# Performance work log

Hardware: AMD Instinct MI355X
Metric: run time of the kernel (lower is better)

The kernel has to match this reference:

```python
import jax, jax.numpy as jnp
import numpy as np

B, L, P, K, D, H = 8192, 224, 6, 5, 128, 4
S = K * K                 # 25 spatial positions in the patch
CENTER = S // 2           # central target pixel index
SCALE_RANGE = 0.2
BN_EPS = 1e-5


def _uniform(k, shape, fan_in):
    s = 1.0 / np.sqrt(fan_in)
    return jax.random.uniform(k, shape, jnp.float32, -s, s)


def setup_inputs() -> dict:
    key = jax.random.key(0)
    ks = jax.random.split(key, 32)
    inp = {}
    inp["x"] = jax.random.normal(ks[0], (B, L, K, K), jnp.float32)
    # attention projections (stored as (in, out), applied as x @ W + b)
    inp["wk_w"] = _uniform(ks[1], (L, D), L); inp["wk_b"] = _uniform(ks[2], (D,), L)
    inp["wv_w"] = _uniform(ks[3], (L, D), L); inp["wv_b"] = _uniform(ks[4], (D,), L)
    inp["wq_w"] = _uniform(ks[5], (L, D), L); inp["wq_b"] = _uniform(ks[6], (D,), L)
    inp["ng_w"] = _uniform(ks[7], (D, 1), D); inp["ng_b"] = _uniform(ks[8], (1,), D)
    # ffn branch: GLU(128->64) -> BN -> GLU(64->P)
    inp["f1_fw"] = _uniform(ks[9], (D, 64), D);  inp["f1_fb"] = _uniform(ks[10], (64,), D)
    inp["f1_gw"] = _uniform(ks[11], (D, 64), D); inp["f1_gb"] = _uniform(ks[12], (64,), D)
    inp["f_bn_g"] = jnp.ones((64,), jnp.float32); inp["f_bn_b"] = jnp.zeros((64,), jnp.float32)
    inp["f2_fw"] = _uniform(ks[13], (64, P), 64); inp["f2_fb"] = _uniform(ks[14], (P,), 64)
    inp["f2_gw"] = _uniform(ks[15], (64, P), 64); inp["f2_gb"] = _uniform(ks[16], (P,), 64)
    # scalar branch: same shapes
    inp["s1_fw"] = _uniform(ks[17], (D, 64), D);  inp["s1_fb"] = _uniform(ks[18], (64,), D)
    inp["s1_gw"] = _uniform(ks[19], (D, 64), D);  inp["s1_gb"] = _uniform(ks[20], (64,), D)
    inp["s_bn_g"] = jnp.ones((64,), jnp.float32); inp["s_bn_b"] = jnp.zeros((64,), jnp.float32)
    inp["s2_fw"] = _uniform(ks[21], (64, P), 64); inp["s2_fb"] = _uniform(ks[22], (P,), 64)
    inp["s2_gw"] = _uniform(ks[23], (64, P), 64); inp["s2_gb"] = _uniform(ks[24], (P,), 64)
    # endmember spectra (P, L), nonnegative as typical for HSI
    inp["endmember"] = jax.random.uniform(ks[25], (P, L), jnp.float32)
    return inp


def _swish(x):
    return x * jax.nn.sigmoid(x)


def _glu(x, fw, fb, gw, gb):
    return (x @ fw + fb) * jax.nn.sigmoid(x @ gw + gb)


def _bn_train(x, g, b):
    # BatchNorm1d training-mode forward: biased batch stats over batch dim
    m = jnp.mean(x, axis=0)
    v = jnp.var(x, axis=0)
    return (x - m) * jax.lax.rsqrt(v + BN_EPS) * g + b


def _forward(x, wk_w, wk_b, wv_w, wv_b, wq_w, wq_b, ng_w, ng_b,
             f1_fw, f1_fb, f1_gw, f1_gb, f_bn_g, f_bn_b, f2_fw, f2_fb, f2_gw, f2_gb,
             s1_fw, s1_fb, s1_gw, s1_gb, s_bn_g, s_bn_b, s2_fw, s2_fb, s2_gw, s2_gb,
             endmember):
    b = x.shape[0]
    xt = x.reshape(b, L, S).transpose(0, 2, 1)        # (B, S, L)
    keys = xt @ wk_w + wk_b                            # (B, S, D)
    vals = xt @ wv_w + wv_b                            # (B, S, D)
    q = xt[:, CENTER] @ wq_w + wq_b                    # (B, D)
    dk, dv = D // H, D // H
    kh = keys.reshape(b, S, H, dk)
    qh = q.reshape(b, H, dk)
    # note: scaling uses full key_dim (np.sqrt(self.key_dim)), not per-head dim
    scores = jnp.einsum('bhd,bshd->bhs', qh, kh) / np.sqrt(D).astype(np.float32)
    mask = jnp.zeros((S,), jnp.float32).at[CENTER].set(-1e6)
    att = jax.nn.softmax(scores + mask, axis=-1)       # (B, H, S)
    vh = vals.reshape(b, S, H, dv)
    surround = jnp.einsum('bhs,bshd->bhd', att, vh).reshape(b, D)
    central = vals[:, CENTER]                          # (B, D)
    nearby = jax.nn.sigmoid((central - surround) @ ng_w + ng_b)  # (B, 1)
    ss = central + nearby * surround                   # (B, D) spatial-spectral feature

    h = _glu(_swish(ss), f1_fw, f1_fb, f1_gw, f1_gb)
    h = _swish(_bn_train(h, f_bn_g, f_bn_b))
    abd = jax.nn.softmax(_glu(h, f2_fw, f2_fb, f2_gw, f2_gb), axis=1)  # (B, P)

    g = _glu(_swish(ss), s1_fw, s1_fb, s1_gw, s1_gb)
    g = _swish(_bn_train(g, s_bn_g, s_bn_b))
    edm_scale = jnp.tanh(_glu(g, s2_fw, s2_fb, s2_gw, s2_gb))          # (B, P)

    scale = 1.0 + SCALE_RANGE * edm_scale[:, :, None]  # (B, P, 1)
    edm = scale * endmember[None]                      # (B, P, L)
    recon = jnp.einsum('bp,bpl->bl', abd, edm)         # (B, L)
    return recon, abd, edm_scale


def reference(x, wk_w, wk_b, wv_w, wv_b, wq_w, wq_b, ng_w, ng_b,
              f1_fw, f1_fb, f1_gw, f1_gb, f_bn_g, f_bn_b, f2_fw, f2_fb, f2_gw, f2_gb,
              s1_fw, s1_fb, s1_gw, s1_gb, s_bn_g, s_bn_b, s2_fw, s2_fb, s2_gw, s2_gb,
              endmember):
    return _forward(x, wk_w, wk_b, wv_w, wv_b, wq_w, wq_b, ng_w, ng_b,
                    f1_fw, f1_fb, f1_gw, f1_gb, f_bn_g, f_bn_b, f2_fw, f2_fb, f2_gw, f2_gb,
                    s1_fw, s1_fb, s1_gw, s1_gb, s_bn_g, s_bn_b, s2_fw, s2_fb, s2_gw, s2_gb,
                    endmember)
```

## Files before the change

kernel.cpp:

```cpp
#include <hip/hip_runtime.h>
#include <hip/hip_bf16.h>

typedef unsigned short ushort;
typedef unsigned int   uint;
typedef __bf16 bfrag_t __attribute__((ext_vector_type(8)));
typedef float  ffrag_t __attribute__((ext_vector_type(4)));

#define NB   8192
#define LL   224
#define SS   25
#define CTR  12
#define DD   128
#define PP   6
#define HID  64
#define GPB  2
#define NGRP 4
#define NKC  7
#define NMT  4
#define NNT  24
#define VST  132
#define VBASE (GPB * SS * VST)
#define WPK_ELEMS (NKC * NNT * 64 * 8)
#define FC1_ELEMS (4 * 16 * 64 * 8)

__device__ __forceinline__ float f_sigmoid(float x) { return 1.0f / (1.0f + __expf(-x)); }
__device__ __forceinline__ ushort f2bf(float f) {
    __hip_bfloat16 h = __float2bfloat16(f);
    ushort u; __builtin_memcpy(&u, &h, 2); return u;
}
__device__ __forceinline__ float bfu2f(ushort u) {
    uint v = ((uint)u) << 16; float f; __builtin_memcpy(&f, &v, 4); return f;
}

__global__ __launch_bounds__(256) void k0_pack(
    const float* __restrict__ wk_w, const float* __restrict__ wv_w,
    const float* __restrict__ wq_w,
    const float* __restrict__ f1_fw, const float* __restrict__ f1_gw,
    const float* __restrict__ s1_fw, const float* __restrict__ s1_gw,
    ushort* __restrict__ wpack, ushort* __restrict__ fc1pack,
    float* __restrict__ stats)
{
    const int blk = blockIdx.x;
    if (blk == 0) stats[threadIdx.x] = 0.f;
    if (blk < NNT) {
        const int nt  = blk;
        const int mat = nt >> 3;
        const float* w = mat == 0 ? wk_w : (mat == 1 ? wv_w : wq_w);
        const int cb = (nt & 7) * 16;
        for (int e = threadIdx.x; e < NKC * 64 * 8; e += 256) {
            int j    = e & 7;
            int lane = (e >> 3) & 63;
            int kc   = e >> 9;
            int k = kc * 32 + ((lane >> 4) << 3) + j;
            int c = cb + (lane & 15);
            wpack[((kc * NNT + nt) * 64 + lane) * 8 + j] = f2bf(w[k * DD + c]);
        }
    } else {
        const int nt = blk - NNT;
        const int m2 = nt >> 2;
        const float* w = m2 == 0 ? f1_fw : (m2 == 1 ? f1_gw : (m2 == 2 ? s1_fw : s1_gw));
        const int cb = (nt & 3) * 16;
        for (int e = threadIdx.x; e < 4 * 64 * 8; e += 256) {
            int j    = e & 7;
            int lane = (e >> 3) & 63;
            int kc   = e >> 9;
            int k = kc * 32 + ((lane >> 4) << 3) + j;
            int c = cb + (lane & 15);
            fc1pack[((kc * 16 + nt) * 64 + lane) * 8 + j] = f2bf(w[k * HID + c]);
        }
    }
}

__global__ __launch_bounds__(512, 2) void kA_front(
    const float* __restrict__ x,
    const ushort* __restrict__ wpack,
    const float* __restrict__ wk_b, const float* __restrict__ wv_b,
    const float* __restrict__ wq_b,
    const float* __restrict__ ng_w, const float* __restrict__ ng_b,
    ushort* __restrict__ swv_ws)
{
    __shared__ ushort alds[NMT * NKC * 64 * 8];
    __shared__ float  qv[GPB * DD];
    __shared__ float  att[8 * 26];
    __shared__ float  red[4];

    const int t    = threadIdx.x;
    const int wave = t >> 6;
    const int lane = t & 63;

    const int cC = wave * 16 + (lane & 15);
    const float biask = wk_b[cC];
    const float biasv = wv_b[cC];
    const float biasq = wq_b[cC];
    const float ngw   = ng_w[t & 127];

    float4 xf[6];
    {
        const float4* xb4 = (const float4*)(x + (size_t)(blockIdx.x * NGRP) * GPB * (LL * SS));
#pragma unroll
        for (int k = 0; k < 6; ++k) {
            int q = t + k * 512;
            if (q < 2800) xf[k] = xb4[q];
        }
    }

    for (int j = 0; j < NGRP; ++j) {
        const int b0 = (blockIdx.x * NGRP + j) * GPB;

#pragma unroll
        for (int k = 0; k < 6; ++k) {
            int q = t + k * 512;
            if (q < 2800) {
                int e0 = q * 4;
                int g  = e0 >= 5600;
                int eb0 = e0 - g * 5600;
                int l0 = eb0 / 25;
                int s0 = eb0 - l0 * 25;
#pragma unroll
                for (int c = 0; c < 4; ++c) {
                    int s = s0 + c;
                    int l = l0;
                    if (s >= 25) { s -= 25; ++l; }
                    int r = g * 32 + s;
                    int idx = (((r >> 4) * NKC + (l >> 5)) * 64 +
                               ((r & 15) | (((l >> 3) & 3) << 4))) * 8 + (l & 7);
                    float fv = c == 0 ? xf[k].x : c == 1 ? xf[k].y : c == 2 ? xf[k].z : xf[k].w;
                    alds[idx] = f2bf(fv);
                }
            }
        }
        __syncthreads();

        ffrag_t acck[NMT], accv[NMT], accq[2];
#pragma unroll
        for (int mt = 0; mt < NMT; ++mt) {
            acck[mt] = ffrag_t{0.f, 0.f, 0.f, 0.f};
            accv[mt] = ffrag_t{0.f, 0.f, 0.f, 0.f};
        }
        accq[0] = ffrag_t{0.f, 0.f, 0.f, 0.f};
        accq[1] = ffrag_t{0.f, 0.f, 0.f, 0.f};

        bfrag_t bk = *(const bfrag_t*)(wpack + ((0 * NNT + wave) * 64 + lane) * 8);
        bfrag_t bv = *(const bfrag_t*)(wpack + ((0 * NNT + wave + 8) * 64 + lane) * 8);
        bfrag_t bq = *(const bfrag_t*)(wpack + ((0 * NNT + wave + 16) * 64 + lane) * 8);
#pragma unroll
        for (int kc = 0; kc < NKC; ++kc) {
            bfrag_t nbk, nbv, nbq;
            if (kc + 1 < NKC) {
                nbk = *(const bfrag_t*)(wpack + (((kc + 1) * NNT + wave) * 64 + lane) * 8);
                nbv = *(const bfrag_t*)(wpack + (((kc + 1) * NNT + wave + 8) * 64 + lane) * 8);
                nbq = *(const bfrag_t*)(wpack + (((kc + 1) * NNT + wave + 16) * 64 + lane) * 8);
            }
#pragma unroll
            for (int mt = 0; mt < NMT; ++mt) {
                bfrag_t af = *(const bfrag_t*)(alds + ((mt * NKC + kc) * 64 + lane) * 8);
                acck[mt] = __builtin_amdgcn_mfma_f32_16x16x32_bf16(af, bk, acck[mt], 0, 0, 0);
                accv[mt] = __builtin_amdgcn_mfma_f32_16x16x32_bf16(af, bv, accv[mt], 0, 0, 0);
                if ((mt & 1) == 0)
                    accq[mt >> 1] = __builtin_amdgcn_mfma_f32_16x16x32_bf16(af, bq, accq[mt >> 1], 0, 0, 0);
            }
            if (kc + 1 < NKC) { bk = nbk; bv = nbv; bq = nbq; }
        }
        __syncthreads();

        {
#pragma unroll
            for (int mt = 0; mt < NMT; ++mt) {
#pragma unroll
                for (int reg = 0; reg < 4; ++reg) {
                    int r = mt * 16 + ((lane >> 4) << 2) + reg;
                    int g = r >> 5;
                    int s = r & 31;
                    if (s < SS) {
                        alds[(g * SS + s) * VST + cC]         = f2bf(acck[mt][reg] + biask);
                        alds[VBASE + (g * SS + s) * VST + cC] = f2bf(accv[mt][reg] + biasv);
                    }
                }
            }
            if ((lane >> 4) == 3) {
                qv[cC]      = accq[0][0] + biasq;
                qv[DD + cC] = accq[1][0] + biasq;
            }
        }
        __syncthreads();

        if (j + 1 < NGRP) {
            const float4* xb4 = (const float4*)(x + (size_t)(b0 + GPB) * (LL * SS));
#pragma unroll
            for (int k = 0; k < 6; ++k) {
                int q = t + k * 512;
                if (q < 2800) xf[k] = xb4[q];
            }
        }

        {
            const int r    = t >> 6;
            const int g    = r >> 2;
            const int h    = r & 3;
            const int l32  = lane & 31;
            const int half = lane >> 5;
            float part = 0.f;
            if (l32 < SS) {
                const ushort* kr = alds + (g * SS + l32) * VST + h * 32 + half * 16;
                const float*  qr = qv + g * DD + h * 32 + half * 16;
                float a0 = 0.f, a1 = 0.f, a2 = 0.f, a3 = 0.f;
#pragma unroll
                for (int i = 0; i < 16; i += 4) {
                    a0 = fmaf(qr[i + 0], bfu2f(kr[i + 0]), a0);
                    a1 = fmaf(qr[i + 1], bfu2f(kr[i + 1]), a1);
                    a2 = fmaf(qr[i + 2], bfu2f(kr[i + 2]), a2);
                    a3 = fmaf(qr[i + 3], bfu2f(kr[i + 3]), a3);
                }
                part = (a0 + a1) + (a2 + a3);
            }
            part += __shfl_xor(part, 32);
            float sc = -1e30f;
            if (l32 < SS) {
                sc = part * 0.088388347648318447f;
                if (l32 == CTR) sc -= 1e6f;
            }
            float mx = sc;
#pragma unroll
            for (int m = 16; m > 0; m >>= 1) mx = fmaxf(mx, __shfl_xor(mx, m, 32));
            float e = __expf(sc - mx);
            float sum = e;
#pragma unroll
            for (int m = 16; m > 0; m >>= 1) sum += __shfl_xor(sum, m, 32);
            if (half == 0 && l32 < SS) att[r * 26 + l32] = e / sum;
        }
        __syncthreads();

        if (t < 256) {
            const int g = t >> 7;
            const int d = t & 127;
            const int h = d >> 5;
            const ushort* vrow = alds + VBASE + g * SS * VST + d;
            const float* arow = att + (g * 4 + h) * 26;
            float s0 = 0.f, s1 = 0.f;
#pragma unroll
            for (int s = 0; s < 24; s += 2) {
                s0 = fmaf(arow[s],     bfu2f(vrow[s * VST]),       s0);
                s1 = fmaf(arow[s + 1], bfu2f(vrow[(s + 1) * VST]), s1);
            }
            float sur = fmaf(arow[24], bfu2f(vrow[24 * VST]), s0 + s1);
            float cen = bfu2f(vrow[CTR * VST]);
            float term = (cen - sur) * ngw;
#pragma unroll
            for (int off = 32; off > 0; off >>= 1) term += __shfl_down(term, off);
            if (lane == 0) red[wave] = term;
            __syncthreads();
            float tot = red[g * 2] + red[g * 2 + 1] + ng_b[0];
            float nearby = f_sigmoid(tot);
            float ssv = cen + nearby * sur;
            float sw  = ssv * f_sigmoid(ssv);
            swv_ws[(size_t)(b0 + g) * DD + d] = f2bf(sw);
        } else {
            __syncthreads();
        }
    }
}

__global__ __launch_bounds__(256) void kC_fc1(
    const ushort* __restrict__ swv_ws,
    const ushort* __restrict__ fc1pack,
    const float* __restrict__ f1_fb, const float* __restrict__ f1_gb,
    const float* __restrict__ s1_fb, const float* __restrict__ s1_gb,
    float* __restrict__ h1_ws, float* __restrict__ g1_ws,
    float* __restrict__ stats)
{
    const int t    = threadIdx.x;
    const int wave = t >> 6;
    const int lane = t & 63;
    const int m0   = blockIdx.x * 32;
    const int c16  = wave * 16 + (lane & 15);

    const float fb1 = f1_fb[c16], gb1 = f1_gb[c16];
    const float fb2 = s1_fb[c16], gb2 = s1_gb[c16];

    ffrag_t acc[4][2];
#pragma unroll
    for (int ni = 0; ni < 4; ++ni)
#pragma unroll
        for (int mt = 0; mt < 2; ++mt) acc[ni][mt] = ffrag_t{0.f, 0.f, 0.f, 0.f};

#pragma unroll
    for (int kc = 0; kc < 4; ++kc) {
        bfrag_t bf[4];
#pragma unroll
        for (int ni = 0; ni < 4; ++ni) {
            int nt = wave + 4 * ni;
            bf[ni] = *(const bfrag_t*)(fc1pack + ((kc * 16 + nt) * 64 + lane) * 8);
        }
#pragma unroll
        for (int mt = 0; mt < 2; ++mt) {
            bfrag_t af = *(const bfrag_t*)(swv_ws +
                (size_t)(m0 + mt * 16 + (lane & 15)) * DD + kc * 32 + ((lane >> 4) << 3));
#pragma unroll
            for (int ni = 0; ni < 4; ++ni)
                acc[ni][mt] = __builtin_amdgcn_mfma_f32_16x16x32_bf16(af, bf[ni], acc[ni][mt], 0, 0, 0);
        }
    }

    float hs = 0.f, hq = 0.f, gs = 0.f, gq = 0.f;
#pragma unroll
    for (int mt = 0; mt < 2; ++mt) {
#pragma unroll
        for (int reg = 0; reg < 4; ++reg) {
            int m = m0 + mt * 16 + ((lane >> 4) << 2) + reg;
            float hv = (acc[0][mt][reg] + fb1) * f_sigmoid(acc[1][mt][reg] + gb1);
            float gv = (acc[2][mt][reg] + fb2) * f_sigmoid(acc[3][mt][reg] + gb2);
            h1_ws[(size_t)m * HID + c16] = hv;
            g1_ws[(size_t)m * HID + c16] = gv;
            hs += hv; hq = fmaf(hv, hv, hq);
            gs += gv; gq = fmaf(gv, gv, gq);
        }
    }
    hs += __shfl_xor(hs, 16); hs += __shfl_xor(hs, 32);
    hq += __shfl_xor(hq, 16); hq += __shfl_xor(hq, 32);
    gs += __shfl_xor(gs, 16); gs += __shfl_xor(gs, 32);
    gq += __shfl_xor(gq, 16); gq += __shfl_xor(gq, 32);
    const int cg = lane >> 4;
    float val = cg == 0 ? hs : cg == 1 ? hq : cg == 2 ? gs : gq;
    atomicAdd(&stats[cg * 64 + c16], val);
}

#define K3G 16
__global__ __launch_bounds__(256) void k3_back(
    const float* __restrict__ h1, const float* __restrict__ g1,
    const float* __restrict__ stats,
    const float* __restrict__ f_bng, const float* __restrict__ f_bnb,
    const float* __restrict__ s_bng, const float* __restrict__ s_bnb,
    const float* __restrict__ f2_fw, const float* __restrict__ f2_fb,
    const float* __restrict__ f2_gw, const float* __restrict__ f2_gb,
    const float* __restrict__ s2_fw, const float* __restrict__ s2_fb,
    const float* __restrict__ s2_gw, const float* __restrict__ s2_gb,
    const float* __restrict__ endm,
    float* __restrict__ out_recon, float* __restrict__ out_abd,
    float* __restrict__ out_es)
{
    const int B0 = blockIdx.x * K3G;
    const int t = threadIdx.x;
    __shared__ float bnl[256];
    __shared__ float w2[4][HID * PP];
    __shared__ float b2[4][8];
    __shared__ float endl[PP * LL];
    __shared__ float hh[K3G * 65], gg[K3G * 65];
    __shared__ float logit[K3G * 8], esv[K3G * 8], coef[K3G * 8];

    if (t < 128) {
        int br = t >> 6, j = t & 63;
        float S1 = stats[br * 128 + j];
        float S2 = stats[br * 128 + 64 + j];
        float m   = S1 * (1.0f / NB);
        float var = S2 * (1.0f / NB) - m * m;
        float gam = br ? s_bng[j] : f_bng[j];
        float be  = br ? s_bnb[j] : f_bnb[j];
        float a   = gam * rsqrtf(var + 1e-5f);
        bnl[br * 128 + j]      = a;
        bnl[br * 128 + 64 + j] = be - m * a;
    }
    for (int i = t; i < HID * PP; i += 256) {
        w2[0][i] = f2_fw[i];
        w2[1][i] = f2_gw[i];
        w2[2][i] = s2_fw[i];
        w2[3][i] = s2_gw[i];
    }
    if (t < PP) {
        b2[0][t] = f2_fb[t];
        b2[1][t] = f2_gb[t];
        b2[2][t] = s2_fb[t];
        b2[3][t] = s2_gb[t];
    }
    for (int i = t; i < PP * LL; i += 256) endl[i] = endm[i];
    __syncthreads();

    for (int i = t; i < K3G * HID; i += 256) {
        int ba = i >> 6, j = i & 63;
        float v1 = h1[(size_t)(B0 + ba) * HID + j] * bnl[j] + bnl[64 + j];
        hh[ba * 65 + j] = v1 * f_sigmoid(v1);
        float v2 = g1[(size_t)(B0 + ba) * HID + j] * bnl[128 + j] + bnl[192 + j];
        gg[ba * 65 + j] = v2 * f_sigmoid(v2);
    }
    __syncthreads();

    for (int i = t; i < K3G * 2 * PP; i += 256) {
        int ba = i / (2 * PP);
        int rr = i - ba * (2 * PP);
        int br = rr / PP;
        int p  = rr - br * PP;
        const float* src = (br ? gg : hh) + ba * 65;
        const float* fw  = w2[br * 2];
        const float* gw  = w2[br * 2 + 1];
        float df = b2[br * 2][p], dg = b2[br * 2 + 1][p];
#pragma unroll 8
        for (int j = 0; j < HID; ++j) {
            float v = src[j];
            df = fmaf(v, fw[j * PP + p], df);
            dg = fmaf(v, gw[j * PP + p], dg);
        }
        float glu = df * f_sigmoid(dg);
        if (br == 0) {
            logit[ba * 8 + p] = glu;
        } else {
            float e = tanhf(glu);
            esv[ba * 8 + p] = e;
            out_es[(size_t)(B0 + ba) * PP + p] = e;
        }
    }
    __syncthreads();

    if (t < K3G) {
        float mx = -1e30f;
#pragma unroll
        for (int p = 0; p < PP; ++p) mx = fmaxf(mx, logit[t * 8 + p]);
        float e[PP]; float sum = 0.f;
#pragma unroll
        for (int p = 0; p < PP; ++p) { e[p] = __expf(logit[t * 8 + p] - mx); sum += e[p]; }
        float inv = 1.0f / sum;
#pragma unroll
        for (int p = 0; p < PP; ++p) {
            float a = e[p] * inv;
            out_abd[(size_t)(B0 + t) * PP + p] = a;
            coef[t * 8 + p] = a * (1.0f + 0.2f * esv[t * 8 + p]);
        }
    }
    __syncthreads();

    for (int i = t; i < K3G * LL; i += 256) {
        int ba = i / LL;
        int l  = i - ba * LL;
        float r = 0.f;
#pragma unroll
        for (int p = 0; p < PP; ++p)
            r = fmaf(coef[ba * 8 + p], endl[p * LL + l], r);
        out_recon[(size_t)(B0 + ba) * LL + l] = r;
    }
}

extern "C" void kernel_launch(void* const* d_in, const int* in_sizes, int n_in,
                              void* d_out, int out_size, void* d_ws, size_t ws_size,
                              hipStream_t stream)
{
    const float* x     = (const float*)d_in[0];
    const float* wk_w  = (const float*)d_in[1];
    const float* wk_b  = (const float*)d_in[2];
    const float* wv_w  = (const float*)d_in[3];
    const float* wv_b  = (const float*)d_in[4];
    const float* wq_w  = (const float*)d_in[5];
    const float* wq_b  = (const float*)d_in[6];
    const float* ng_w  = (const float*)d_in[7];
    const float* ng_b  = (const float*)d_in[8];
    const float* f1_fw = (const float*)d_in[9];
    const float* f1_fb = (const float*)d_in[10];
    const float* f1_gw = (const float*)d_in[11];
    const float* f1_gb = (const float*)d_in[12];
    const float* f_bng = (const float*)d_in[13];
    const float* f_bnb = (const float*)d_in[14];
    const float* f2_fw = (const float*)d_in[15];
    const float* f2_fb = (const float*)d_in[16];
    const float* f2_gw = (const float*)d_in[17];
    const float* f2_gb = (const float*)d_in[18];
    const float* s1_fw = (const float*)d_in[19];
    const float* s1_fb = (const float*)d_in[20];
    const float* s1_gw = (const float*)d_in[21];
    const float* s1_gb = (const float*)d_in[22];
    const float* s_bng = (const float*)d_in[23];
    const float* s_bnb = (const float*)d_in[24];
    const float* s2_fw = (const float*)d_in[25];
    const float* s2_fb = (const float*)d_in[26];
    const float* s2_gw = (const float*)d_in[27];
    const float* s2_gb = (const float*)d_in[28];
    const float* endm  = (const float*)d_in[29];

    float* ws = (float*)d_ws;
    float*  h1_ws   = ws;
    float*  g1_ws   = ws + (size_t)NB * HID;
    float*  stats   = ws + 1048576;
    ushort* wpack   = (ushort*)(ws + 1048832);
    ushort* fc1pack = (ushort*)(ws + 1048832 + WPK_ELEMS / 2);
    ushort* swv_ws  = (ushort*)(ws + 1048832 + (WPK_ELEMS + FC1_ELEMS) / 2);

    float* out       = (float*)d_out;
    float* out_recon = out;
    float* out_abd   = out + (size_t)NB * LL;
    float* out_es    = out + (size_t)NB * (LL + PP);

    k0_pack<<<NNT + 16, 256, 0, stream>>>(wk_w, wv_w, wq_w, f1_fw, f1_gw,
                                          s1_fw, s1_gw, wpack, fc1pack, stats);
    kA_front<<<NB / (GPB * NGRP), 512, 0, stream>>>(x, wpack, wk_b, wv_b, wq_b,
                                                    ng_w, ng_b, swv_ws);
    kC_fc1<<<NB / 32, 256, 0, stream>>>(swv_ws, fc1pack, f1_fb, f1_gb,
                                        s1_fb, s1_gb, h1_ws, g1_ws, stats);
    k3_back<<<NB / K3G, 256, 0, stream>>>(h1_ws, g1_ws, stats,
                                          f_bng, f_bnb, s_bng, s_bnb,
                                          f2_fw, f2_fb, f2_gw, f2_gb,
                                          s2_fw, s2_fb, s2_gw, s2_gb,
                                          endm, out_recon, out_abd, out_es);
}
```

Before: 358.6 us.

## Double groups per front block, use all waves in surround reduction, halve fc1 tiles

The front kernel now handles 8 groups per block instead of 4, which halves the grid and amortises the bias and weight setup over more batch items. The surround-weighted V sum now runs on all 8 waves instead of the first 4, with each half-wave summing half the spatial positions and combining the halves with a shuffle. The fc1 MFMA kernel drops from 32 to 16 rows per block, doubling its grid and reusing one A fragment per k-chunk. The trade-offs are less parallelism in the front kernel, more atomic stats updates, and repeated weight-fragment loads in fc1.

```diff
diff --git a/kernel.cpp b/kernel.cpp
--- a/kernel.cpp
+++ b/kernel.cpp
@@ -14,7 +14,7 @@
 #define PP   6
 #define HID  64
 #define GPB  2
-#define NGRP 4
+#define NGRP 8
 #define NKC  7
 #define NMT  4
 #define NNT  24
@@ -82,7 +82,7 @@
     __shared__ ushort alds[NMT * NKC * 64 * 8];
     __shared__ float  qv[GPB * DD];
     __shared__ float  att[8 * 26];
-    __shared__ float  red[4];
+    __shared__ float  red[8];
 
     const int t    = threadIdx.x;
     const int wave = t >> 6;
@@ -92,7 +92,9 @@
     const float biask = wk_b[cC];
     const float biasv = wv_b[cC];
     const float biasq = wq_b[cC];
-    const float ngw   = ng_w[t & 127];
+    const int   d4    = ((wave & 3) << 5) | (lane & 31);
+    const float ngw   = ng_w[d4];
+    const float ngb   = ng_b[0];
 
     float4 xf[6];
     {
@@ -230,32 +232,32 @@
         }
         __syncthreads();
 
-        if (t < 256) {
-            const int g = t >> 7;
-            const int d = t & 127;
-            const int h = d >> 5;
-            const ushort* vrow = alds + VBASE + g * SS * VST + d;
-            const float* arow = att + (g * 4 + h) * 26;
-            float s0 = 0.f, s1 = 0.f;
-#pragma unroll
-            for (int s = 0; s < 24; s += 2) {
-                s0 = fmaf(arow[s],     bfu2f(vrow[s * VST]),       s0);
-                s1 = fmaf(arow[s + 1], bfu2f(vrow[(s + 1) * VST]), s1);
-            }
-            float sur = fmaf(arow[24], bfu2f(vrow[24 * VST]), s0 + s1);
+        {
+            const int g    = wave >> 2;
+            const int h    = wave & 3;
+            const int half = lane >> 5;
+            const ushort* vrow = alds + VBASE + g * SS * VST + d4;
+            const float*  arow = att + (g * 4 + h) * 26;
+            float part = 0.f;
+            const int sbeg = half ? 13 : 0;
+            const int send = half ? 25 : 13;
+#pragma unroll
+            for (int s = sbeg; s < send; ++s)
+                part = fmaf(arow[s], bfu2f(vrow[s * VST]), part);
+            float sur = part + __shfl_xor(part, 32);
             float cen = bfu2f(vrow[CTR * VST]);
-            float term = (cen - sur) * ngw;
+            float term = half ? 0.f : (cen - sur) * ngw;
 #pragma unroll
             for (int off = 32; off > 0; off >>= 1) term += __shfl_down(term, off);
             if (lane == 0) red[wave] = term;
             __syncthreads();
-            float tot = red[g * 2] + red[g * 2 + 1] + ng_b[0];
+            float tot = red[(g << 2)] + red[(g << 2) + 1] +
+                        red[(g << 2) + 2] + red[(g << 2) + 3] + ngb;
             float nearby = f_sigmoid(tot);
             float ssv = cen + nearby * sur;
             float sw  = ssv * f_sigmoid(ssv);
-            swv_ws[(size_t)(b0 + g) * DD + d] = f2bf(sw);
-        } else {
-            __syncthreads();
+            if (half == 0)
+                swv_ws[(size_t)(b0 + g) * DD + d4] = f2bf(sw);
         }
     }
 }
@@ -271,49 +273,38 @@
     const int t    = threadIdx.x;
     const int wave = t >> 6;
     const int lane = t & 63;
-    const int m0   = blockIdx.x * 32;
+    const int m0   = blockIdx.x * 16;
     const int c16  = wave * 16 + (lane & 15);
 
     const float fb1 = f1_fb[c16], gb1 = f1_gb[c16];
     const float fb2 = s1_fb[c16], gb2 = s1_gb[c16];
 
-    ffrag_t acc[4][2];
-#pragma unroll
-    for (int ni = 0; ni < 4; ++ni)
-#pragma unroll
-        for (int mt = 0; mt < 2; ++mt) acc[ni][mt] = ffrag_t{0.f, 0.f, 0.f, 0.f};
+    ffrag_t acc[4];
+#pragma unroll
+    for (int ni = 0; ni < 4; ++ni) acc[ni] = ffrag_t{0.f, 0.f, 0.f, 0.f};
 
 #pragma unroll
     for (int kc = 0; kc < 4; ++kc) {
-        bfrag_t bf[4];
+        bfrag_t af = *(const bfrag_t*)(swv_ws +
+            (size_t)(m0 + (lane & 15)) * DD + kc * 32 + ((lane >> 4) << 3));
 #pragma unroll
         for (int ni = 0; ni < 4; ++ni) {
             int nt = wave + 4 * ni;
-            bf[ni] = *(const bfrag_t*)(fc1pack + ((kc * 16 + nt) * 64 + lane) * 8);
-        }
-#pragma unroll
-        for (int mt = 0; mt < 2; ++mt) {
-            bfrag_t af = *(const bfrag_t*)(swv_ws +
-                (size_t)(m0 + mt * 16 + (lane & 15)) * DD + kc * 32 + ((lane >> 4) << 3));
-#pragma unroll
-            for (int ni = 0; ni < 4; ++ni)
-                acc[ni][mt] = __builtin_amdgcn_mfma_f32_16x16x32_bf16(af, bf[ni], acc[ni][mt], 0, 0, 0);
+            bfrag_t bf = *(const bfrag_t*)(fc1pack + ((kc * 16 + nt) * 64 + lane) * 8);
+            acc[ni] = __builtin_amdgcn_mfma_f32_16x16x32_bf16(af, bf, acc[ni], 0, 0, 0);
         }
     }
 
     float hs = 0.f, hq = 0.f, gs = 0.f, gq = 0.f;
 #pragma unroll
-    for (int mt = 0; mt < 2; ++mt) {
-#pragma unroll
-        for (int reg = 0; reg < 4; ++reg) {
-            int m = m0 + mt * 16 + ((lane >> 4) << 2) + reg;
-            float hv = (acc[0][mt][reg] + fb1) * f_sigmoid(acc[1][mt][reg] + gb1);
-            float gv = (acc[2][mt][reg] + fb2) * f_sigmoid(acc[3][mt][reg] + gb2);
-            h1_ws[(size_t)m * HID + c16] = hv;
-            g1_ws[(size_t)m * HID + c16] = gv;
-            hs += hv; hq = fmaf(hv, hv, hq);
-            gs += gv; gq = fmaf(gv, gv, gq);
-        }
+    for (int reg = 0; reg < 4; ++reg) {
+        int m = m0 + ((lane >> 4) << 2) + reg;
+        float hv = (acc[0][reg] + fb1) * f_sigmoid(acc[1][reg] + gb1);
+        float gv = (acc[2][reg] + fb2) * f_sigmoid(acc[3][reg] + gb2);
+        h1_ws[(size_t)m * HID + c16] = hv;
+        g1_ws[(size_t)m * HID + c16] = gv;
+        hs += hv; hq = fmaf(hv, hv, hq);
+        gs += gv; gq = fmaf(gv, gv, gq);
     }
     hs += __shfl_xor(hs, 16); hs += __shfl_xor(hs, 32);
     hq += __shfl_xor(hq, 16); hq += __shfl_xor(hq, 32);
@@ -489,7 +480,7 @@
                                           s1_fw, s1_gw, wpack, fc1pack, stats);
     kA_front<<<NB / (GPB * NGRP), 512, 0, stream>>>(x, wpack, wk_b, wv_b, wq_b,
                                                     ng_w, ng_b, swv_ws);
-    kC_fc1<<<NB / 32, 256, 0, stream>>>(swv_ws, fc1pack, f1_fb, f1_gb,
+    kC_fc1<<<NB / 16, 256, 0, stream>>>(swv_ws, fc1pack, f1_fb, f1_gb,
                                         s1_fb, s1_gb, h1_ws, g1_ws, stats);
     k3_back<<<NB / K3G, 256, 0, stream>>>(h1_ws, g1_ws, stats,
                                           f_bng, f_bnb, s_bng, s_bnb,
```

New measurement: 362.3 us. No clear change (+1.0%).
